# Kernel optimization log

Measured on AMD Instinct MI355X. Metric: run time of the kernel, lower is better.

## Reference

```python
import jax, jax.numpy as jnp
import numpy as np

EDGE_TYPES = 5
D = 256      # input_dim == output_dim
HID = 128    # hard-coded hidden size of agg MLPs


def setup_inputs() -> dict:
    key = jax.random.key(0)
    ks = jax.random.split(key, 8)
    B, E, N = 4, 8000, 2000
    edge_distribution = jax.random.uniform(ks[0], (B, E, EDGE_TYPES), dtype=jnp.float32)
    H = jax.random.normal(ks[1], (B, E, N), dtype=jnp.float32)
    ori = jax.random.normal(ks[2], (B, N, D), dtype=jnp.float32)
    # Stacked per-edge-type MLP params: Linear(D->128), ReLU, Linear(128->D)
    W1 = jax.random.normal(ks[3], (EDGE_TYPES, D, HID), dtype=jnp.float32) * (1.0 / np.sqrt(D))
    b1 = jax.random.normal(ks[4], (EDGE_TYPES, HID), dtype=jnp.float32) * 0.01
    W2 = jax.random.normal(ks[5], (EDGE_TYPES, HID, D), dtype=jnp.float32) * (1.0 / np.sqrt(HID))
    b2 = jax.random.normal(ks[6], (EDGE_TYPES, D), dtype=jnp.float32) * 0.01
    return {"edge_distribution": edge_distribution, "H": H, "ori": ori,
            "W1": W1, "b1": b1, "W2": W2, "b2": b2}


def reference(edge_distribution, H, ori, W1, b1, W2, b2):
    # edges = H @ ori : [B, E, D]
    edges = jnp.matmul(H, ori)
    # Per-edge-type 2-layer MLP, vectorized over the type axis t
    h = jax.nn.relu(jnp.einsum('bed,tdh->tbeh', edges, W1) + b1[:, None, None, :])  # [T,B,E,HID]
    mlp_out = jnp.einsum('tbeh,thd->tbed', h, W2) + b2[:, None, None, :]            # [T,B,E,D]
    # Gated accumulate: sum_t edge_distribution[...,t] * mlp_out[t]
    edge_feature = jnp.einsum('bet,tbed->bed', edge_distribution, mlp_out)          # [B,E,D]
    # node_feature = concat(H^T @ edge_feature, ori)
    node_feature = jnp.concatenate(
        [jnp.matmul(jnp.swapaxes(H, 1, 2), edge_feature), ori], axis=-1)            # [B,N,2D]
    return node_feature
```

## Files before the change

### kernel.cpp

```cpp
#include <hip/hip_runtime.h>

typedef unsigned short u16;
typedef short bf16x8 __attribute__((ext_vector_type(8)));
typedef float f32x4 __attribute__((ext_vector_type(4)));
typedef unsigned short u16x8 __attribute__((ext_vector_type(8)));

#define GLL16(gp, lp) __builtin_amdgcn_global_load_lds( \
    (__attribute__((address_space(1))) const unsigned int*)(gp), \
    (__attribute__((address_space(3))) unsigned int*)(lp), 16, 0, 0)

static __device__ __forceinline__ u16 f2bf(float f){
  unsigned u = __builtin_bit_cast(unsigned, f);
  u += 0x7fffu + ((u >> 16) & 1u);
  return (u16)(u >> 16);
}

__global__ void transpose_f32(const float* __restrict__ src, u16* __restrict__ dst,
                              int R, int C, int Rpad, long sB, long dB){
  __shared__ u16 tile[32][33];
  const int b = blockIdx.z;
  src += (long)b*sB; dst += (long)b*dB;
  const int r0 = blockIdx.x*32, c0 = blockIdx.y*32;
  const int j = threadIdx.x & 31, i0 = threadIdx.x >> 5;
  #pragma unroll
  for (int ii=0; ii<32; ii+=8){
    int r = r0+i0+ii, c = c0+j;
    u16 v = 0;
    if (r < R && c < C) v = f2bf(src[(long)r*C + c]);
    tile[i0+ii][j] = v;
  }
  __syncthreads();
  #pragma unroll
  for (int ii=0; ii<32; ii+=8){
    int c = c0+i0+ii, r = r0+j;
    if (c < C && r < Rpad) dst[(long)c*Rpad + r] = tile[j][i0+ii];
  }
}

__global__ void transpose_u16(const u16* __restrict__ src, u16* __restrict__ dst,
                              int R, int C, int Rpad, long sB, long dB){
  __shared__ u16 tile[32][33];
  const int b = blockIdx.z;
  src += (long)b*sB; dst += (long)b*dB;
  const int r0 = blockIdx.x*32, c0 = blockIdx.y*32;
  const int j = threadIdx.x & 31, i0 = threadIdx.x >> 5;
  #pragma unroll
  for (int ii=0; ii<32; ii+=8){
    int r = r0+i0+ii, c = c0+j;
    u16 v = 0;
    if (r < R && c < C) v = src[(long)r*C + c];
    tile[i0+ii][j] = v;
  }
  __syncthreads();
  #pragma unroll
  for (int ii=0; ii<32; ii+=8){
    int c = c0+i0+ii, r = r0+j;
    if (c < C && r < Rpad) dst[(long)c*Rpad + r] = tile[j][i0+ii];
  }
}

__global__ __launch_bounds__(256,3) void g1_kernel(
    const float* __restrict__ Hm, const u16* __restrict__ oriT,
    u16* __restrict__ edges, u16* __restrict__ HT){
  __shared__ u16 As[2][64*32];
  __shared__ u16 Bs[2][256*32];
  __shared__ u16 At[2][32*66];
  const int b = blockIdx.y, bm = blockIdx.x*64;
  const int tid = threadIdx.x;
  const int w = tid>>6, quad = (tid&63)>>4, l16 = tid&15;
  const int wn = w*64;
  const float* Ab = Hm + (size_t)b*8000*2000 + (size_t)bm*2000;
  const u16*  Bb = oriT + (size_t)b*256*2048;
  u16* HTb = HT + (size_t)b*2048*8000;

  float4 pa[2];
  auto loadA = [&](int kt){
    const int k0 = kt*32;
    #pragma unroll
    for (int i=0;i<2;i++){
      int idx = i*256+tid, row = idx>>3, c4 = (idx&7)*4;
      bool ok = (k0+c4 < 2000);
      pa[i] = ok ? *(const float4*)(Ab + (size_t)row*2000 + k0+c4) : make_float4(0.f,0.f,0.f,0.f);
    }
  };
  auto storeA = [&](int kt){
    const int buf = kt&1;
    #pragma unroll
    for (int i=0;i<2;i++){
      int idx = i*256+tid, row = idx>>3, c4 = (idx&7)*4;
      ushort4 o; o.x=f2bf(pa[i].x); o.y=f2bf(pa[i].y); o.z=f2bf(pa[i].z); o.w=f2bf(pa[i].w);
      *(ushort4*)(&As[buf][idx*4]) = o;
      At[buf][(c4+0)*66 + row] = o.x;
      At[buf][(c4+1)*66 + row] = o.y;
      At[buf][(c4+2)*66 + row] = o.z;
      At[buf][(c4+3)*66 + row] = o.w;
    }
  };
  auto stageB = [&](int kt){
    const int buf = kt&1, k0 = kt*32;
    #pragma unroll
    for (int i=0;i<4;i++){
      int idx = i*256+tid, row = idx>>2, c8 = (idx&3)*8;
      GLL16(Bb + (size_t)row*2048 + k0+c8, &Bs[buf][(i*256 + w*64)*8]);
    }
  };

  f32x4 acc[4][4];
  #pragma unroll
  for (int i=0;i<4;i++)
    #pragma unroll
    for (int j=0;j<4;j++) acc[i][j] = (f32x4){0.f,0.f,0.f,0.f};

  loadA(0); stageB(0);
  for (int kt=0; kt<63; kt++){
    storeA(kt);
    __syncthreads();
    if (kt+1 < 63){ loadA(kt+1); stageB(kt+1); }
    const int buf = kt&1, k0 = kt*32;
    {
      int kk = tid>>3, c = tid&7, m0 = c*8;
      u16x8 v = *(const u16x8*)(&At[buf][kk*66 + m0]);
      *(u16x8*)(HTb + (size_t)(k0+kk)*8000 + bm + m0) = v;
    }
    bf16x8 af[4], bf[4];
    #pragma unroll
    for (int mi=0;mi<4;mi++) af[mi] = *(const bf16x8*)(&As[buf][(mi*16+l16)*32 + quad*8]);
    #pragma unroll
    for (int ni=0;ni<4;ni++) bf[ni] = *(const bf16x8*)(&Bs[buf][(wn+ni*16+l16)*32 + quad*8]);
    #pragma unroll
    for (int mi=0;mi<4;mi++)
      #pragma unroll
      for (int ni=0;ni<4;ni++)
        acc[mi][ni] = __builtin_amdgcn_mfma_f32_16x16x32_bf16(af[mi], bf[ni], acc[mi][ni], 0,0,0);
  }
  #pragma unroll
  for (int mi=0;mi<4;mi++){
    #pragma unroll
    for (int r=0;r<4;r++){
      int gm = bm + mi*16 + quad*4 + r;
      u16* dst = edges + ((size_t)b*8000 + gm)*256;
      #pragma unroll
      for (int ni=0;ni<4;ni++) dst[wn + ni*16 + l16] = f2bf(acc[mi][ni][r]);
    }
  }
}

__global__ __launch_bounds__(256,2) void m1_kernel(
    const u16* __restrict__ edges, const u16* __restrict__ W1T,
    const float* __restrict__ b1, const float* __restrict__ edist, u16* __restrict__ H1){
  __shared__ u16 As[2][128*32];
  __shared__ u16 Bs[2][128*32];
  __shared__ float eds[128], b1s[128];
  const int t = blockIdx.y, bm = blockIdx.x*128;
  const int tid = threadIdx.x;
  const int w = tid>>6, quad = (tid&63)>>4, l16 = tid&15;
  const int wm = (w&1)*64, wn = (w>>1)*64;
  if (tid < 128){ eds[tid] = edist[(size_t)(bm+tid)*5 + t]; b1s[tid] = b1[t*128+tid]; }
  const u16* Ab = edges + (size_t)bm*256;
  const u16* Bb = W1T + (size_t)t*128*256;

  auto stage = [&](int kt){
    const int buf = kt&1, k0 = kt*32;
    #pragma unroll
    for (int i=0;i<2;i++){
      int idx = i*256+tid, row = idx>>2, c8 = (idx&3)*8;
      GLL16(Ab + (size_t)row*256 + k0+c8, &As[buf][(i*256 + w*64)*8]);
      GLL16(Bb + (size_t)row*256 + k0+c8, &Bs[buf][(i*256 + w*64)*8]);
    }
  };

  f32x4 acc[4][4];
  #pragma unroll
  for (int i=0;i<4;i++)
    #pragma unroll
    for (int j=0;j<4;j++) acc[i][j] = (f32x4){0.f,0.f,0.f,0.f};

  stage(0);
  for (int kt=0; kt<8; kt++){
    __syncthreads();
    if (kt+1 < 8) stage(kt+1);
    const int buf = kt&1;
    bf16x8 af[4], bf[4];
    #pragma unroll
    for (int mi=0;mi<4;mi++) af[mi] = *(const bf16x8*)(&As[buf][(wm+mi*16+l16)*32 + quad*8]);
    #pragma unroll
    for (int ni=0;ni<4;ni++) bf[ni] = *(const bf16x8*)(&Bs[buf][(wn+ni*16+l16)*32 + quad*8]);
    #pragma unroll
    for (int mi=0;mi<4;mi++)
      #pragma unroll
      for (int ni=0;ni<4;ni++)
        acc[mi][ni] = __builtin_amdgcn_mfma_f32_16x16x32_bf16(af[mi], bf[ni], acc[mi][ni], 0,0,0);
  }
  #pragma unroll
  for (int mi=0;mi<4;mi++){
    #pragma unroll
    for (int r=0;r<4;r++){
      int lrow = wm + mi*16 + quad*4 + r;
      float s = eds[lrow];
      u16* dst = H1 + ((size_t)t*32000 + bm + lrow)*128;
      #pragma unroll
      for (int ni=0;ni<4;ni++){
        int lc = wn + ni*16 + l16;
        float v = fmaxf(acc[mi][ni][r] + b1s[lc], 0.f) * s;
        dst[lc] = f2bf(v);
      }
    }
  }
}

__global__ __launch_bounds__(256,2) void m2_kernel(
    const u16* __restrict__ H1, const u16* __restrict__ W2T,
    const float* __restrict__ b2, const float* __restrict__ edist, u16* __restrict__ EF){
  __shared__ u16 As[2][128*32];
  __shared__ u16 Bs[2][128*32];
  __shared__ float eds[640], b2s[640];
  const int bm = blockIdx.x*128, bn = blockIdx.y*128;
  const int tid = threadIdx.x;
  const int w = tid>>6, quad = (tid&63)>>4, l16 = tid&15;
  const int wm = (w&1)*64, wn = (w>>1)*64;
  for (int i=tid;i<640;i+=256){
    eds[i] = edist[(size_t)bm*5 + i];
    b2s[i] = b2[(i>>7)*256 + bn + (i&127)];
  }
  auto stage = [&](int kt){
    const int buf = kt&1, t = kt>>2, k0 = (kt&3)*32;
    #pragma unroll
    for (int i=0;i<2;i++){
      int idx = i*256+tid, row = idx>>2, c8 = (idx&3)*8;
      GLL16(H1 + ((size_t)t*32000 + bm+row)*128 + k0+c8, &As[buf][(i*256 + w*64)*8]);
      GLL16(W2T + ((size_t)t*256 + bn+row)*128 + k0+c8, &Bs[buf][(i*256 + w*64)*8]);
    }
  };

  f32x4 acc[4][4];
  #pragma unroll
  for (int i=0;i<4;i++)
    #pragma unroll
    for (int j=0;j<4;j++) acc[i][j] = (f32x4){0.f,0.f,0.f,0.f};

  stage(0);
  for (int kt=0; kt<20; kt++){
    __syncthreads();
    if (kt+1 < 20) stage(kt+1);
    const int buf = kt&1;
    bf16x8 af[4], bf[4];
    #pragma unroll
    for (int mi=0;mi<4;mi++) af[mi] = *(const bf16x8*)(&As[buf][(wm+mi*16+l16)*32 + quad*8]);
    #pragma unroll
    for (int ni=0;ni<4;ni++) bf[ni] = *(const bf16x8*)(&Bs[buf][(wn+ni*16+l16)*32 + quad*8]);
    #pragma unroll
    for (int mi=0;mi<4;mi++)
      #pragma unroll
      for (int ni=0;ni<4;ni++)
        acc[mi][ni] = __builtin_amdgcn_mfma_f32_16x16x32_bf16(af[mi], bf[ni], acc[mi][ni], 0,0,0);
  }
  #pragma unroll
  for (int mi=0;mi<4;mi++){
    #pragma unroll
    for (int r=0;r<4;r++){
      int lrow = wm + mi*16 + quad*4 + r;
      float e0=eds[lrow*5+0], e1=eds[lrow*5+1], e2=eds[lrow*5+2], e3=eds[lrow*5+3], e4=eds[lrow*5+4];
      u16* dst = EF + (size_t)(bm+lrow)*256 + bn;
      #pragma unroll
      for (int ni=0;ni<4;ni++){
        int lc = wn + ni*16 + l16;
        float bias = e0*b2s[lc] + e1*b2s[128+lc] + e2*b2s[256+lc] + e3*b2s[384+lc] + e4*b2s[512+lc];
        dst[lc] = f2bf(acc[mi][ni][r] + bias);
      }
    }
  }
}

__global__ __launch_bounds__(256,3) void g3_kernel(
    const u16* __restrict__ HT, const u16* __restrict__ EFt, float* __restrict__ part){
  __shared__ u16 As[2][64*32];
  __shared__ u16 Bs[2][256*32];
  const int bm = blockIdx.x*64, ks = blockIdx.y, b = blockIdx.z;
  const int tid = threadIdx.x;
  const int w = tid>>6, quad = (tid&63)>>4, l16 = tid&15;
  const int wn = w*64;
  const u16* Ab = HT + (size_t)b*2048*8000 + (size_t)bm*8000;
  const u16* Bb = EFt + (size_t)b*256*8000;
  const int it0 = (250*ks)/4, it1 = (250*(ks+1))/4;

  auto stage = [&](int kt){
    const int buf = kt&1, k0 = kt*32;
    {
      int row = tid>>2, c8 = (tid&3)*8;
      GLL16(Ab + (size_t)row*8000 + k0+c8, &As[buf][(w*64)*8]);
    }
    #pragma unroll
    for (int i=0;i<4;i++){
      int idx = i*256+tid, row = idx>>2, c8 = (idx&3)*8;
      GLL16(Bb + (size_t)row*8000 + k0+c8, &Bs[buf][(i*256 + w*64)*8]);
    }
  };

  f32x4 acc[4][4];
  #pragma unroll
  for (int i=0;i<4;i++)
    #pragma unroll
    for (int j=0;j<4;j++) acc[i][j] = (f32x4){0.f,0.f,0.f,0.f};

  stage(it0);
  for (int kt=it0; kt<it1; kt++){
    __syncthreads();
    if (kt+1 < it1) stage(kt+1);
    const int buf = kt&1;
    bf16x8 af[4], bf[4];
    #pragma unroll
    for (int mi=0;mi<4;mi++) af[mi] = *(const bf16x8*)(&As[buf][(mi*16+l16)*32 + quad*8]);
    #pragma unroll
    for (int ni=0;ni<4;ni++) bf[ni] = *(const bf16x8*)(&Bs[buf][(wn+ni*16+l16)*32 + quad*8]);
    #pragma unroll
    for (int mi=0;mi<4;mi++)
      #pragma unroll
      for (int ni=0;ni<4;ni++)
        acc[mi][ni] = __builtin_amdgcn_mfma_f32_16x16x32_bf16(af[mi], bf[ni], acc[mi][ni], 0,0,0);
  }
  float* dst0 = part + ((size_t)(b*4 + ks)*2048)*256;
  #pragma unroll
  for (int mi=0;mi<4;mi++){
    #pragma unroll
    for (int r=0;r<4;r++){
      int gm = bm + mi*16 + quad*4 + r;
      float* dst = dst0 + (size_t)gm*256;
      #pragma unroll
      for (int ni=0;ni<4;ni++) dst[wn + ni*16 + l16] = acc[mi][ni][r];
    }
  }
}

__global__ void assemble_kernel(const float* __restrict__ part, const float* __restrict__ ori,
                                float* __restrict__ out){
  const int b = blockIdx.y;
  int u = blockIdx.x*256 + threadIdx.x;
  int n = u>>6, c4 = (u&63)*4;
  f32x4 s = (f32x4){0.f,0.f,0.f,0.f};
  #pragma unroll
  for (int ks=0; ks<4; ks++)
    s += *(const f32x4*)(part + ((size_t)(b*4+ks)*2048 + n)*256 + c4);
  float* dst = out + ((size_t)(b*2000+n))*512;
  *(f32x4*)(dst + c4) = s;
  *(f32x4*)(dst + 256 + c4) = *(const f32x4*)(ori + ((size_t)(b*2000+n))*256 + c4);
}

extern "C" void kernel_launch(void* const* d_in, const int* in_sizes, int n_in,
                              void* d_out, int out_size, void* d_ws, size_t ws_size,
                              hipStream_t stream) {
  const float* ed  = (const float*)d_in[0];
  const float* Hm  = (const float*)d_in[1];
  const float* ori = (const float*)d_in[2];
  const float* W1  = (const float*)d_in[3];
  const float* b1  = (const float*)d_in[4];
  const float* W2  = (const float*)d_in[5];
  const float* b2  = (const float*)d_in[6];
  float* out = (float*)d_out;
  char* ws = (char*)d_ws;

  u16* HT    = (u16*)(ws);
  u16* oriT  = (u16*)(ws + 131072000);
  u16* W1T   = (u16*)(ws + 135266304);
  u16* W2T   = (u16*)(ws + 135593984);
  u16* edges = (u16*)(ws + 135921664);
  u16* H1    = (u16*)(ws + 152305664);
  u16* EF    = (u16*)(ws + 193265664);
  u16* EFt   = edges;
  float* part = (float*)H1;

  hipLaunchKernelGGL(transpose_f32, dim3(64,8,4), dim3(256), 0, stream,
                     ori, oriT, 2000, 256, 2048, 512000L, 524288L);
  hipLaunchKernelGGL(transpose_f32, dim3(8,4,5), dim3(256), 0, stream,
                     W1, W1T, 256, 128, 256, 32768L, 32768L);
  hipLaunchKernelGGL(transpose_f32, dim3(4,8,5), dim3(256), 0, stream,
                     W2, W2T, 128, 256, 128, 32768L, 32768L);

  hipLaunchKernelGGL(g1_kernel, dim3(125,4), dim3(256), 0, stream, Hm, oriT, edges, HT);
  hipLaunchKernelGGL(m1_kernel, dim3(250,5), dim3(256), 0, stream, edges, W1T, b1, ed, H1);
  hipLaunchKernelGGL(m2_kernel, dim3(250,2), dim3(256), 0, stream, H1, W2T, b2, ed, EF);
  hipLaunchKernelGGL(transpose_u16, dim3(250,8,4), dim3(256), 0, stream,
                     EF, EFt, 8000, 256, 8000, 2048000L, 2048000L);
  hipLaunchKernelGGL(g3_kernel, dim3(32,4,4), dim3(256), 0, stream, HT, EFt, part);
  hipLaunchKernelGGL(assemble_kernel, dim3(500,4), dim3(256), 0, stream, part, ori, out);

  (void)in_sizes; (void)n_in; (void)ws_size;
}
```

Baseline: 594.9 us.

## Fuse per-type MLP layers into one kernel and deepen K-steps in GEMMs

Replaces the separate m1 and m2 kernels with a single m12 kernel that keeps a 64-row edge tile in LDS, computes each edge type's hidden activations, and feeds them straight into the second layer. This removes the H1 intermediate's round trip through global memory and one launch. The g1 and g3 GEMMs now process two 32-wide K sub-tiles per barrier, which halves the number of synchronisations but doubles LDS use and lowers occupancy (launch bounds 1 and 2). The fused kernel runs only 500 blocks of 4 waves and stages weights with plain loads, so latency may be poorly hidden.

```diff
diff --git a/kernel.cpp b/kernel.cpp
--- a/kernel.cpp
+++ b/kernel.cpp
@@ -59,12 +59,12 @@
   }
 }
 
-__global__ __launch_bounds__(256,3) void g1_kernel(
+__global__ __launch_bounds__(256,1) void g1_kernel(
     const float* __restrict__ Hm, const u16* __restrict__ oriT,
     u16* __restrict__ edges, u16* __restrict__ HT){
-  __shared__ u16 As[2][64*32];
-  __shared__ u16 Bs[2][256*32];
-  __shared__ u16 At[2][32*66];
+  __shared__ u16 As[2][2][64*32];
+  __shared__ u16 Bs[2][2][256*32];
+  __shared__ u16 At[2][2][32*66];
   const int b = blockIdx.y, bm = blockIdx.x*64;
   const int tid = threadIdx.x;
   const int w = tid>>6, quad = (tid&63)>>4, l16 = tid&15;
@@ -73,35 +73,39 @@
   const u16*  Bb = oriT + (size_t)b*256*2048;
   u16* HTb = HT + (size_t)b*2048*8000;
 
-  float4 pa[2];
-  auto loadA = [&](int kt){
-    const int k0 = kt*32;
-    #pragma unroll
-    for (int i=0;i<2;i++){
-      int idx = i*256+tid, row = idx>>3, c4 = (idx&7)*4;
+  float4 pa[4];
+  auto loadA = [&](int s){
+    const int k0 = s*64;
+    #pragma unroll
+    for (int i=0;i<4;i++){
+      int idx = i*256+tid, row = idx>>4, c4 = (idx&15)*4;
       bool ok = (k0+c4 < 2000);
       pa[i] = ok ? *(const float4*)(Ab + (size_t)row*2000 + k0+c4) : make_float4(0.f,0.f,0.f,0.f);
     }
   };
-  auto storeA = [&](int kt){
-    const int buf = kt&1;
-    #pragma unroll
-    for (int i=0;i<2;i++){
-      int idx = i*256+tid, row = idx>>3, c4 = (idx&7)*4;
+  auto storeA = [&](int s){
+    const int buf = s&1;
+    #pragma unroll
+    for (int i=0;i<4;i++){
+      int idx = i*256+tid, row = idx>>4, c4 = (idx&15)*4;
+      int sub = c4>>5, cc = c4&31;
       ushort4 o; o.x=f2bf(pa[i].x); o.y=f2bf(pa[i].y); o.z=f2bf(pa[i].z); o.w=f2bf(pa[i].w);
-      *(ushort4*)(&As[buf][idx*4]) = o;
-      At[buf][(c4+0)*66 + row] = o.x;
-      At[buf][(c4+1)*66 + row] = o.y;
-      At[buf][(c4+2)*66 + row] = o.z;
-      At[buf][(c4+3)*66 + row] = o.w;
-    }
-  };
-  auto stageB = [&](int kt){
-    const int buf = kt&1, k0 = kt*32;
-    #pragma unroll
-    for (int i=0;i<4;i++){
-      int idx = i*256+tid, row = idx>>2, c8 = (idx&3)*8;
-      GLL16(Bb + (size_t)row*2048 + k0+c8, &Bs[buf][(i*256 + w*64)*8]);
+      *(ushort4*)(&As[buf][sub][row*32 + cc]) = o;
+      At[buf][sub][(cc+0)*66 + row] = o.x;
+      At[buf][sub][(cc+1)*66 + row] = o.y;
+      At[buf][sub][(cc+2)*66 + row] = o.z;
+      At[buf][sub][(cc+3)*66 + row] = o.w;
+    }
+  };
+  auto stageB = [&](int s){
+    const int buf = s&1, k0 = s*64;
+    #pragma unroll
+    for (int sub=0; sub<2; sub++){
+      #pragma unroll
+      for (int i=0;i<4;i++){
+        int idx = i*256+tid, row = idx>>2, c8 = (idx&3)*8;
+        GLL16(Bb + (size_t)row*2048 + k0 + sub*32 + c8, &Bs[buf][sub][(i*256 + w*64)*8]);
+      }
     }
   };
 
@@ -112,26 +116,29 @@
     for (int j=0;j<4;j++) acc[i][j] = (f32x4){0.f,0.f,0.f,0.f};
 
   loadA(0); stageB(0);
-  for (int kt=0; kt<63; kt++){
-    storeA(kt);
+  for (int s=0; s<32; s++){
+    storeA(s);
     __syncthreads();
-    if (kt+1 < 63){ loadA(kt+1); stageB(kt+1); }
-    const int buf = kt&1, k0 = kt*32;
-    {
-      int kk = tid>>3, c = tid&7, m0 = c*8;
-      u16x8 v = *(const u16x8*)(&At[buf][kk*66 + m0]);
-      *(u16x8*)(HTb + (size_t)(k0+kk)*8000 + bm + m0) = v;
-    }
-    bf16x8 af[4], bf[4];
-    #pragma unroll
-    for (int mi=0;mi<4;mi++) af[mi] = *(const bf16x8*)(&As[buf][(mi*16+l16)*32 + quad*8]);
-    #pragma unroll
-    for (int ni=0;ni<4;ni++) bf[ni] = *(const bf16x8*)(&Bs[buf][(wn+ni*16+l16)*32 + quad*8]);
-    #pragma unroll
-    for (int mi=0;mi<4;mi++)
-      #pragma unroll
-      for (int ni=0;ni<4;ni++)
-        acc[mi][ni] = __builtin_amdgcn_mfma_f32_16x16x32_bf16(af[mi], bf[ni], acc[mi][ni], 0,0,0);
+    if (s+1 < 32){ stageB(s+1); loadA(s+1); }
+    const int buf = s&1, k0 = s*64;
+    #pragma unroll
+    for (int sub=0; sub<2; sub++){
+      {
+        int kk = tid>>3, m0 = (tid&7)*8;
+        u16x8 v = *(const u16x8*)(&At[buf][sub][kk*66 + m0]);
+        *(u16x8*)(HTb + (size_t)(k0 + sub*32 + kk)*8000 + bm + m0) = v;
+      }
+      bf16x8 af[4], bf[4];
+      #pragma unroll
+      for (int mi=0;mi<4;mi++) af[mi] = *(const bf16x8*)(&As[buf][sub][(mi*16+l16)*32 + quad*8]);
+      #pragma unroll
+      for (int ni=0;ni<4;ni++) bf[ni] = *(const bf16x8*)(&Bs[buf][sub][(wn+ni*16+l16)*32 + quad*8]);
+      #pragma unroll
+      for (int mi=0;mi<4;mi++)
+        #pragma unroll
+        for (int ni=0;ni<4;ni++)
+          acc[mi][ni] = __builtin_amdgcn_mfma_f32_16x16x32_bf16(af[mi], bf[ni], acc[mi][ni], 0,0,0);
+    }
   }
   #pragma unroll
   for (int mi=0;mi<4;mi++){
@@ -145,154 +152,138 @@
   }
 }
 
-__global__ __launch_bounds__(256,2) void m1_kernel(
-    const u16* __restrict__ edges, const u16* __restrict__ W1T,
-    const float* __restrict__ b1, const float* __restrict__ edist, u16* __restrict__ H1){
-  __shared__ u16 As[2][128*32];
-  __shared__ u16 Bs[2][128*32];
-  __shared__ float eds[128], b1s[128];
-  const int t = blockIdx.y, bm = blockIdx.x*128;
+__global__ __launch_bounds__(256,1) void m12_kernel(
+    const u16* __restrict__ edges, const u16* __restrict__ W1T, const u16* __restrict__ W2T,
+    const float* __restrict__ b1, const float* __restrict__ b2,
+    const float* __restrict__ edist, u16* __restrict__ EF){
+  __shared__ u16 Es[8][64*32];
+  __shared__ u16 Hs[4][64*32];
+  __shared__ u16 Ws1[2][128*32];
+  __shared__ u16 Ws2[2][256*32];
+  __shared__ float eds[64*5], b1s[640], b2s[1280];
+  const int bm = blockIdx.x*64;
   const int tid = threadIdx.x;
   const int w = tid>>6, quad = (tid&63)>>4, l16 = tid&15;
-  const int wm = (w&1)*64, wn = (w>>1)*64;
-  if (tid < 128){ eds[tid] = edist[(size_t)(bm+tid)*5 + t]; b1s[tid] = b1[t*128+tid]; }
-  const u16* Ab = edges + (size_t)bm*256;
-  const u16* Bb = W1T + (size_t)t*128*256;
-
-  auto stage = [&](int kt){
-    const int buf = kt&1, k0 = kt*32;
-    #pragma unroll
-    for (int i=0;i<2;i++){
-      int idx = i*256+tid, row = idx>>2, c8 = (idx&3)*8;
-      GLL16(Ab + (size_t)row*256 + k0+c8, &As[buf][(i*256 + w*64)*8]);
-      GLL16(Bb + (size_t)row*256 + k0+c8, &Bs[buf][(i*256 + w*64)*8]);
-    }
-  };
-
-  f32x4 acc[4][4];
-  #pragma unroll
-  for (int i=0;i<4;i++)
-    #pragma unroll
-    for (int j=0;j<4;j++) acc[i][j] = (f32x4){0.f,0.f,0.f,0.f};
-
-  stage(0);
-  for (int kt=0; kt<8; kt++){
-    __syncthreads();
-    if (kt+1 < 8) stage(kt+1);
-    const int buf = kt&1;
-    bf16x8 af[4], bf[4];
-    #pragma unroll
-    for (int mi=0;mi<4;mi++) af[mi] = *(const bf16x8*)(&As[buf][(wm+mi*16+l16)*32 + quad*8]);
-    #pragma unroll
-    for (int ni=0;ni<4;ni++) bf[ni] = *(const bf16x8*)(&Bs[buf][(wn+ni*16+l16)*32 + quad*8]);
-    #pragma unroll
-    for (int mi=0;mi<4;mi++)
-      #pragma unroll
-      for (int ni=0;ni<4;ni++)
-        acc[mi][ni] = __builtin_amdgcn_mfma_f32_16x16x32_bf16(af[mi], bf[ni], acc[mi][ni], 0,0,0);
-  }
-  #pragma unroll
-  for (int mi=0;mi<4;mi++){
-    #pragma unroll
-    for (int r=0;r<4;r++){
-      int lrow = wm + mi*16 + quad*4 + r;
-      float s = eds[lrow];
-      u16* dst = H1 + ((size_t)t*32000 + bm + lrow)*128;
-      #pragma unroll
-      for (int ni=0;ni<4;ni++){
-        int lc = wn + ni*16 + l16;
-        float v = fmaxf(acc[mi][ni][r] + b1s[lc], 0.f) * s;
-        dst[lc] = f2bf(v);
-      }
-    }
-  }
-}
-
-__global__ __launch_bounds__(256,2) void m2_kernel(
-    const u16* __restrict__ H1, const u16* __restrict__ W2T,
-    const float* __restrict__ b2, const float* __restrict__ edist, u16* __restrict__ EF){
-  __shared__ u16 As[2][128*32];
-  __shared__ u16 Bs[2][128*32];
-  __shared__ float eds[640], b2s[640];
-  const int bm = blockIdx.x*128, bn = blockIdx.y*128;
-  const int tid = threadIdx.x;
-  const int w = tid>>6, quad = (tid&63)>>4, l16 = tid&15;
-  const int wm = (w&1)*64, wn = (w>>1)*64;
-  for (int i=tid;i<640;i+=256){
-    eds[i] = edist[(size_t)bm*5 + i];
-    b2s[i] = b2[(i>>7)*256 + bn + (i&127)];
-  }
-  auto stage = [&](int kt){
-    const int buf = kt&1, t = kt>>2, k0 = (kt&3)*32;
-    #pragma unroll
-    for (int i=0;i<2;i++){
-      int idx = i*256+tid, row = idx>>2, c8 = (idx&3)*8;
-      GLL16(H1 + ((size_t)t*32000 + bm+row)*128 + k0+c8, &As[buf][(i*256 + w*64)*8]);
-      GLL16(W2T + ((size_t)t*256 + bn+row)*128 + k0+c8, &Bs[buf][(i*256 + w*64)*8]);
-    }
-  };
-
-  f32x4 acc[4][4];
-  #pragma unroll
-  for (int i=0;i<4;i++)
-    #pragma unroll
-    for (int j=0;j<4;j++) acc[i][j] = (f32x4){0.f,0.f,0.f,0.f};
-
-  stage(0);
-  for (int kt=0; kt<20; kt++){
-    __syncthreads();
-    if (kt+1 < 20) stage(kt+1);
-    const int buf = kt&1;
-    bf16x8 af[4], bf[4];
-    #pragma unroll
-    for (int mi=0;mi<4;mi++) af[mi] = *(const bf16x8*)(&As[buf][(wm+mi*16+l16)*32 + quad*8]);
-    #pragma unroll
-    for (int ni=0;ni<4;ni++) bf[ni] = *(const bf16x8*)(&Bs[buf][(wn+ni*16+l16)*32 + quad*8]);
-    #pragma unroll
-    for (int mi=0;mi<4;mi++)
-      #pragma unroll
-      for (int ni=0;ni<4;ni++)
-        acc[mi][ni] = __builtin_amdgcn_mfma_f32_16x16x32_bf16(af[mi], bf[ni], acc[mi][ni], 0,0,0);
-  }
-  #pragma unroll
-  for (int mi=0;mi<4;mi++){
-    #pragma unroll
-    for (int r=0;r<4;r++){
-      int lrow = wm + mi*16 + quad*4 + r;
-      float e0=eds[lrow*5+0], e1=eds[lrow*5+1], e2=eds[lrow*5+2], e3=eds[lrow*5+3], e4=eds[lrow*5+4];
-      u16* dst = EF + (size_t)(bm+lrow)*256 + bn;
-      #pragma unroll
-      for (int ni=0;ni<4;ni++){
-        int lc = wn + ni*16 + l16;
-        float bias = e0*b2s[lc] + e1*b2s[128+lc] + e2*b2s[256+lc] + e3*b2s[384+lc] + e4*b2s[512+lc];
-        dst[lc] = f2bf(acc[mi][ni][r] + bias);
-      }
-    }
-  }
-}
-
-__global__ __launch_bounds__(256,3) void g3_kernel(
+  const int r0 = w*16;
+
+  for (int i=tid;i<320;i+=256)  eds[i] = edist[(size_t)bm*5 + i];
+  for (int i=tid;i<640;i+=256)  b1s[i] = b1[i];
+  for (int i=tid;i<1280;i+=256) b2s[i] = b2[i];
+  {
+    int row = tid>>2, cp = tid&3;
+    const u16* src = edges + ((size_t)(bm+row))*256 + cp*64;
+    #pragma unroll
+    for (int j=0;j<8;j++){
+      u16x8 v = *(const u16x8*)(src + j*8);
+      *(u16x8*)(&Es[cp*2 + (j>>2)][row*32 + (j&3)*8]) = v;
+    }
+  }
+
+  auto stageW1 = [&](int t, int ks){
+    const int buf = ks&1;
+    int row = tid>>1, p = tid&1;
+    const u16* src = W1T + ((size_t)(t*128+row))*256 + ks*32;
+    #pragma unroll
+    for (int j=0;j<2;j++){
+      int ch = p*2 + j;
+      u16x8 v = *(const u16x8*)(src + ch*8);
+      *(u16x8*)(&Ws1[buf][row*32 + ch*8]) = v;
+    }
+  };
+  auto stageW2 = [&](int t, int ks){
+    const int buf = ks&1;
+    int row = tid;
+    const u16* src = W2T + ((size_t)(t*256+row))*128 + ks*32;
+    #pragma unroll
+    for (int j=0;j<4;j++){
+      u16x8 v = *(const u16x8*)(src + j*8);
+      *(u16x8*)(&Ws2[buf][row*32 + j*8]) = v;
+    }
+  };
+
+  f32x4 acc2[16];
+  #pragma unroll
+  for (int i=0;i<16;i++) acc2[i] = (f32x4){0.f,0.f,0.f,0.f};
+
+  for (int t=0; t<5; t++){
+    f32x4 acc1[8];
+    #pragma unroll
+    for (int i=0;i<8;i++) acc1[i] = (f32x4){0.f,0.f,0.f,0.f};
+    stageW1(t, 0);
+    for (int ks=0; ks<8; ks++){
+      __syncthreads();
+      if (ks+1 < 8) stageW1(t, ks+1);
+      const int buf = ks&1;
+      bf16x8 af = *(const bf16x8*)(&Es[ks][(r0+l16)*32 + quad*8]);
+      #pragma unroll
+      for (int ni=0;ni<8;ni++){
+        bf16x8 bf = *(const bf16x8*)(&Ws1[buf][(ni*16+l16)*32 + quad*8]);
+        acc1[ni] = __builtin_amdgcn_mfma_f32_16x16x32_bf16(af, bf, acc1[ni], 0,0,0);
+      }
+    }
+    #pragma unroll
+    for (int ni=0;ni<8;ni++){
+      int col = ni*16 + l16;
+      #pragma unroll
+      for (int r=0;r<4;r++){
+        int row = r0 + quad*4 + r;
+        float v = fmaxf(acc1[ni][r] + b1s[t*128+col], 0.f) * eds[row*5+t];
+        Hs[ni>>1][row*32 + (ni&1)*16 + l16] = f2bf(v);
+      }
+    }
+    stageW2(t, 0);
+    for (int ks=0; ks<4; ks++){
+      __syncthreads();
+      if (ks+1 < 4) stageW2(t, ks+1);
+      const int buf = ks&1;
+      bf16x8 af = *(const bf16x8*)(&Hs[ks][(r0+l16)*32 + quad*8]);
+      #pragma unroll
+      for (int ni=0;ni<16;ni++){
+        bf16x8 bf = *(const bf16x8*)(&Ws2[buf][(ni*16+l16)*32 + quad*8]);
+        acc2[ni] = __builtin_amdgcn_mfma_f32_16x16x32_bf16(af, bf, acc2[ni], 0,0,0);
+      }
+    }
+  }
+  #pragma unroll
+  for (int r=0;r<4;r++){
+    int row = r0 + quad*4 + r;
+    float e0=eds[row*5+0], e1=eds[row*5+1], e2=eds[row*5+2], e3=eds[row*5+3], e4=eds[row*5+4];
+    u16* dst = EF + ((size_t)(bm+row))*256;
+    #pragma unroll
+    for (int ni=0;ni<16;ni++){
+      int d = ni*16 + l16;
+      float bias = e0*b2s[d] + e1*b2s[256+d] + e2*b2s[512+d] + e3*b2s[768+d] + e4*b2s[1024+d];
+      dst[d] = f2bf(acc2[ni][r] + bias);
+    }
+  }
+}
+
+__global__ __launch_bounds__(256,2) void g3_kernel(
     const u16* __restrict__ HT, const u16* __restrict__ EFt, float* __restrict__ part){
-  __shared__ u16 As[2][64*32];
-  __shared__ u16 Bs[2][256*32];
+  __shared__ u16 As[2][2][64*32];
+  __shared__ u16 Bs[2][2][256*32];
   const int bm = blockIdx.x*64, ks = blockIdx.y, b = blockIdx.z;
   const int tid = threadIdx.x;
   const int w = tid>>6, quad = (tid&63)>>4, l16 = tid&15;
   const int wn = w*64;
   const u16* Ab = HT + (size_t)b*2048*8000 + (size_t)bm*8000;
   const u16* Bb = EFt + (size_t)b*256*8000;
-  const int it0 = (250*ks)/4, it1 = (250*(ks+1))/4;
-
-  auto stage = [&](int kt){
-    const int buf = kt&1, k0 = kt*32;
-    {
-      int row = tid>>2, c8 = (tid&3)*8;
-      GLL16(Ab + (size_t)row*8000 + k0+c8, &As[buf][(w*64)*8]);
-    }
-    #pragma unroll
-    for (int i=0;i<4;i++){
-      int idx = i*256+tid, row = idx>>2, c8 = (idx&3)*8;
-      GLL16(Bb + (size_t)row*8000 + k0+c8, &Bs[buf][(i*256 + w*64)*8]);
+  const int r32[5] = {0,64,128,192,250};
+  const int s0 = r32[ks]>>1, s1 = r32[ks+1]>>1;
+
+  auto stage = [&](int s){
+    const int buf = s&1, k0 = s*64;
+    #pragma unroll
+    for (int sub=0; sub<2; sub++){
+      {
+        int row = tid>>2, c8 = (tid&3)*8;
+        GLL16(Ab + (size_t)row*8000 + k0 + sub*32 + c8, &As[buf][sub][(w*64)*8]);
+      }
+      #pragma unroll
+      for (int i=0;i<4;i++){
+        int idx = i*256+tid, row = idx>>2, c8 = (idx&3)*8;
+        GLL16(Bb + (size_t)row*8000 + k0 + sub*32 + c8, &Bs[buf][sub][(i*256 + w*64)*8]);
+      }
     }
   };
 
@@ -302,21 +293,24 @@
     #pragma unroll
     for (int j=0;j<4;j++) acc[i][j] = (f32x4){0.f,0.f,0.f,0.f};
 
-  stage(it0);
-  for (int kt=it0; kt<it1; kt++){
+  stage(s0);
+  for (int s=s0; s<s1; s++){
     __syncthreads();
-    if (kt+1 < it1) stage(kt+1);
-    const int buf = kt&1;
-    bf16x8 af[4], bf[4];
-    #pragma unroll
-    for (int mi=0;mi<4;mi++) af[mi] = *(const bf16x8*)(&As[buf][(mi*16+l16)*32 + quad*8]);
-    #pragma unroll
-    for (int ni=0;ni<4;ni++) bf[ni] = *(const bf16x8*)(&Bs[buf][(wn+ni*16+l16)*32 + quad*8]);
-    #pragma unroll
-    for (int mi=0;mi<4;mi++)
-      #pragma unroll
-      for (int ni=0;ni<4;ni++)
-        acc[mi][ni] = __builtin_amdgcn_mfma_f32_16x16x32_bf16(af[mi], bf[ni], acc[mi][ni], 0,0,0);
+    if (s+1 < s1) stage(s+1);
+    const int buf = s&1;
+    #pragma unroll
+    for (int sub=0; sub<2; sub++){
+      bf16x8 af[4], bf[4];
+      #pragma unroll
+      for (int mi=0;mi<4;mi++) af[mi] = *(const bf16x8*)(&As[buf][sub][(mi*16+l16)*32 + quad*8]);
+      #pragma unroll
+      for (int ni=0;ni<4;ni++) bf[ni] = *(const bf16x8*)(&Bs[buf][sub][(wn+ni*16+l16)*32 + quad*8]);
+      #pragma unroll
+      for (int mi=0;mi<4;mi++)
+        #pragma unroll
+        for (int ni=0;ni<4;ni++)
+          acc[mi][ni] = __builtin_amdgcn_mfma_f32_16x16x32_bf16(af[mi], bf[ni], acc[mi][ni], 0,0,0);
+    }
   }
   float* dst0 = part + ((size_t)(b*4 + ks)*2048)*256;
   #pragma unroll
@@ -376,8 +370,8 @@
                      W2, W2T, 128, 256, 128, 32768L, 32768L);
 
   hipLaunchKernelGGL(g1_kernel, dim3(125,4), dim3(256), 0, stream, Hm, oriT, edges, HT);
-  hipLaunchKernelGGL(m1_kernel, dim3(250,5), dim3(256), 0, stream, edges, W1T, b1, ed, H1);
-  hipLaunchKernelGGL(m2_kernel, dim3(250,2), dim3(256), 0, stream, H1, W2T, b2, ed, EF);
+  hipLaunchKernelGGL(m12_kernel, dim3(500), dim3(256), 0, stream,
+                     edges, W1T, W2T, b1, b2, ed, EF);
   hipLaunchKernelGGL(transpose_u16, dim3(250,8,4), dim3(256), 0, stream,
                      EF, EFt, 8000, 256, 8000, 2048000L, 2048000L);
   hipLaunchKernelGGL(g3_kernel, dim3(32,4,4), dim3(256), 0, stream, HT, EFt, part);
```

Result: slower. 645.2 us (+8.5%).
